# Optimization experiments

Measured on AMD Instinct MI355X. Metric: run time of the kernel, lower is better.

## Reference

```python
import jax, jax.numpy as jnp
import numpy as np

G = 2000      # number of genes
T = 64        # num_tf
NUM_GOS = 500
GO_DIM = 6
N_OUT = 7
B = 64        # batch (cells)


def _gene_layout():
    num_peaks = (np.arange(G) % 16) + 3          # ragged widths, total 21000
    gene_ids = np.repeat(np.arange(G), num_peaks).astype(np.int32)
    return num_peaks, gene_ids


def setup_inputs() -> dict:
    num_peaks, gene_ids = _gene_layout()
    P = int(num_peaks.sum())                     # 21000 total peaks
    key = jax.random.key(0)
    ks = jax.random.split(key, 7)
    x = jax.random.normal(ks[0], (B, T, P), dtype=jnp.float32)
    # per-peak-per-TF weights: concat of all subNet fc1 weights (each gene's
    # Linear(num_peak*num_tf, 1) is just a dot over its (tf, peak) block)
    W_peaks = jax.random.normal(ks[1], (P, T), dtype=jnp.float32) * 0.02
    b_genes = jax.random.normal(ks[2], (G,), dtype=jnp.float32) * 0.02
    W1 = jax.random.normal(ks[3], (G, NUM_GOS * GO_DIM), dtype=jnp.float32) * 0.02
    b1 = jax.random.normal(ks[4], (NUM_GOS * GO_DIM,), dtype=jnp.float32) * 0.02
    W2 = jax.random.normal(ks[5], (NUM_GOS * GO_DIM, N_OUT), dtype=jnp.float32) * 0.02
    b2 = jax.random.normal(ks[6], (N_OUT,), dtype=jnp.float32) * 0.02
    return {"x": x, "W_peaks": W_peaks, "b_genes": b_genes,
            "W1": W1, "b1": b1, "W2": W2, "b2": b2,
            "gene_ids": jnp.asarray(gene_ids)}


def reference(x, W_peaks, b_genes, W1, b1, W2, b2, gene_ids):
    # per-peak contribution: sum over TFs  -> [B, P]
    per_peak = jnp.einsum('btp,pt->bp', x, W_peaks)
    # ragged per-gene reduction (the subNet loop) -> [B, G]
    x_cat_pre = jax.ops.segment_sum(per_peak.T, gene_ids, num_segments=G).T + b_genes
    x_cat = jax.nn.relu(x_cat_pre)
    h = jax.nn.relu(x_cat @ W1 + b1)             # [B, num_gos*go_dim]
    out = h @ W2 + b2                            # [B, 7]
    return (x_cat, h, out)
```

## Files before the change

kernel.cpp:

```cpp
#include <hip/hip_runtime.h>

#define G_GENES 2000
#define T_TF    64
#define P_PEAKS 21000
#define B_BATCH 64
#define H_DIM   3000
#define N_OUT   7

#define WS_XCAT 0
#define WS_HACC 128000
#define WS_WT   320000


__global__ __launch_bounds__(256) void transpose_w(const float* __restrict__ W,
                                                   float* __restrict__ Wt) {
    __shared__ float tile[64][65];
    const int pBase = blockIdx.x * 64;
    const int tid = threadIdx.x;
    const int lane = tid & 63;
    const int grp  = tid >> 6;
#pragma unroll
    for (int i = 0; i < 16; ++i) {
        int pr = grp + i * 4;
        int p  = pBase + pr;
        if (p < P_PEAKS) tile[pr][lane] = W[(size_t)p * T_TF + lane];
    }
    __syncthreads();
#pragma unroll
    for (int i = 0; i < 16; ++i) {
        int tr = grp + i * 4;
        int p  = pBase + lane;
        if (p < P_PEAKS) Wt[(size_t)tr * P_PEAKS + p] = tile[lane][tr];
    }
}

__global__ __launch_bounds__(256) void peak_dot(const float* __restrict__ x,
                                                const float* __restrict__ Wt,
                                                const int*   __restrict__ gene_ids,
                                                float* __restrict__ xcat_acc) {
    const int p4 = blockIdx.x * 256 + threadIdx.x;
    if (p4 >= P_PEAKS / 4) return;
    const int b = blockIdx.y;
    const int p = p4 * 4;

    const float4* __restrict__ xp = (const float4*)(x + (size_t)b * T_TF * P_PEAKS + p);
    const float4* __restrict__ wp = (const float4*)(Wt + p);
    const int stride4 = P_PEAKS / 4;

    float4 acc = make_float4(0.f, 0.f, 0.f, 0.f);
#pragma unroll 8
    for (int t = 0; t < T_TF; ++t) {
        float4 xv = xp[(size_t)t * stride4];
        float4 wv = wp[(size_t)t * stride4];
        acc.x += xv.x * wv.x;
        acc.y += xv.y * wv.y;
        acc.z += xv.z * wv.z;
        acc.w += xv.w * wv.w;
    }

    const int4 g = *(const int4*)(gene_ids + p);
    float* dst = xcat_acc + (size_t)b * G_GENES;
    float s = acc.x; int cg = g.x;
    if (g.y == cg) s += acc.y; else { atomicAdd(dst + cg, s); cg = g.y; s = acc.y; }
    if (g.z == cg) s += acc.z; else { atomicAdd(dst + cg, s); cg = g.z; s = acc.z; }
    if (g.w == cg) s += acc.w; else { atomicAdd(dst + cg, s); cg = g.w; s = acc.w; }
    atomicAdd(dst + cg, s);
}

__global__ __launch_bounds__(256) void bias_relu_xcat(const float* __restrict__ acc,
                                                      const float* __restrict__ b_genes,
                                                      float* __restrict__ out) {
    int i = blockIdx.x * 256 + threadIdx.x;
    if (i >= B_BATCH * G_GENES) return;
    float v = acc[i] + b_genes[i % G_GENES];
    out[i] = v > 0.f ? v : 0.f;
}

#define KSPLIT 4
#define KCH    (2000 / KSPLIT)
#define KK_CH  20
__global__ __launch_bounds__(256) void gemm1(const float* __restrict__ A,
                                             const float* __restrict__ W1,
                                             float* __restrict__ h_acc) {
    __shared__ __align__(16) float As[KK_CH][64];
    const int tid = threadIdx.x;
    const int tx = tid & 15;
    const int ty = tid >> 4;
    const int colBase = blockIdx.x * 64;
    const int col0 = colBase + tx * 4;
    const int row0 = ty * 4;
    const int k0 = blockIdx.y * KCH;
    const bool colOK = (col0 < H_DIM);

    float4 acc4[4];
#pragma unroll
    for (int r = 0; r < 4; ++r) acc4[r] = make_float4(0.f, 0.f, 0.f, 0.f);

    for (int kc = 0; kc < KCH; kc += KK_CH) {
        __syncthreads();
#pragma unroll
        for (int i = 0; i < 5; ++i) {
            int idx = tid + i * 256;
            int kk = idx >> 6;
            int r  = idx & 63;
            As[kk][r] = A[(size_t)r * G_GENES + k0 + kc + kk];
        }
        __syncthreads();
        if (colOK) {
#pragma unroll
            for (int kk = 0; kk < KK_CH; ++kk) {
                float4 a4 = *(const float4*)&As[kk][row0];
                float4 w4 = *(const float4*)&W1[(size_t)(k0 + kc + kk) * H_DIM + col0];
                acc4[0].x += a4.x * w4.x; acc4[0].y += a4.x * w4.y;
                acc4[0].z += a4.x * w4.z; acc4[0].w += a4.x * w4.w;
                acc4[1].x += a4.y * w4.x; acc4[1].y += a4.y * w4.y;
                acc4[1].z += a4.y * w4.z; acc4[1].w += a4.y * w4.w;
                acc4[2].x += a4.z * w4.x; acc4[2].y += a4.z * w4.y;
                acc4[2].z += a4.z * w4.z; acc4[2].w += a4.z * w4.w;
                acc4[3].x += a4.w * w4.x; acc4[3].y += a4.w * w4.y;
                acc4[3].z += a4.w * w4.z; acc4[3].w += a4.w * w4.w;
            }
        }
    }
    if (colOK) {
#pragma unroll
        for (int r = 0; r < 4; ++r) {
            float* dst = h_acc + (size_t)(row0 + r) * H_DIM + col0;
            atomicAdd(dst + 0, acc4[r].x);
            atomicAdd(dst + 1, acc4[r].y);
            atomicAdd(dst + 2, acc4[r].z);
            atomicAdd(dst + 3, acc4[r].w);
        }
    }
}

__global__ __launch_bounds__(256) void bias_relu_h(const float* __restrict__ acc,
                                                   const float* __restrict__ b1,
                                                   float* __restrict__ out) {
    int i = blockIdx.x * 256 + threadIdx.x;
    if (i >= B_BATCH * H_DIM) return;
    float v = acc[i] + b1[i % H_DIM];
    out[i] = v > 0.f ? v : 0.f;
}

__global__ __launch_bounds__(256) void gemm2(const float* __restrict__ h,
                                             const float* __restrict__ W2,
                                             const float* __restrict__ b2,
                                             float* __restrict__ out) {
    const int b = blockIdx.x;
    const int tid = threadIdx.x;
    float acc[N_OUT];
#pragma unroll
    for (int o = 0; o < N_OUT; ++o) acc[o] = 0.f;
    for (int k = tid; k < H_DIM; k += 256) {
        float hv = h[(size_t)b * H_DIM + k];
#pragma unroll
        for (int o = 0; o < N_OUT; ++o) acc[o] += hv * W2[k * N_OUT + o];
    }
    __shared__ float red[N_OUT][256];
#pragma unroll
    for (int o = 0; o < N_OUT; ++o) red[o][tid] = acc[o];
    __syncthreads();
    for (int s = 128; s > 0; s >>= 1) {
        if (tid < s) {
#pragma unroll
            for (int o = 0; o < N_OUT; ++o) red[o][tid] += red[o][tid + s];
        }
        __syncthreads();
    }
    if (tid < N_OUT) out[(size_t)b * N_OUT + tid] = red[tid][0] + b2[tid];
}

extern "C" void kernel_launch(void* const* d_in, const int* in_sizes, int n_in,
                              void* d_out, int out_size, void* d_ws, size_t ws_size,
                              hipStream_t stream) {
    const float* x       = (const float*)d_in[0];
    const float* W_peaks = (const float*)d_in[1];
    const float* b_genes = (const float*)d_in[2];
    const float* W1      = (const float*)d_in[3];
    const float* b1      = (const float*)d_in[4];
    const float* W2      = (const float*)d_in[5];
    const float* b2      = (const float*)d_in[6];
    const int*   gene_ids = (const int*)d_in[7];

    float* ws = (float*)d_ws;
    float* xcat_acc = ws + WS_XCAT;
    float* h_acc    = ws + WS_HACC;
    float* Wt       = ws + WS_WT;

    float* out_xcat = (float*)d_out;
    float* out_h    = (float*)d_out + 128000;
    float* out_fin  = (float*)d_out + 320000;

    hipMemsetAsync(ws, 0, (size_t)(128000 + 192000) * sizeof(float), stream);

    transpose_w<<<(P_PEAKS + 63) / 64, 256, 0, stream>>>(W_peaks, Wt);

    dim3 g1((P_PEAKS / 4 + 255) / 256, B_BATCH);
    peak_dot<<<g1, 256, 0, stream>>>(x, Wt, gene_ids, xcat_acc);

    bias_relu_xcat<<<(B_BATCH * G_GENES + 255) / 256, 256, 0, stream>>>(
        xcat_acc, b_genes, out_xcat);

    dim3 g2((H_DIM + 63) / 64, KSPLIT);
    gemm1<<<g2, 256, 0, stream>>>(out_xcat, W1, h_acc);

    bias_relu_h<<<(B_BATCH * H_DIM + 255) / 256, 256, 0, stream>>>(
        h_acc, b1, out_h);

    gemm2<<<B_BATCH, 256, 0, stream>>>(out_h, W2, b2, out_fin);
}
```

Measured before the change: 573.5 us.

## Reuse W across 4 batches in peak_dot, transpose xcat for gemm1, raise K-split

peak_dot now gives each thread 4 batch rows, so each Wt load is reused four times and fewer blocks are launched. bias_relu_xcat also writes a transposed [G,B] copy of x_cat, which gives gemm1 coalesced shared-memory tile loads instead of strided ones. gemm1's K split goes from 4 to 8 with a 25-deep chunk, adding parallelism at the cost of more atomics on h_acc. The dominant cost is streaming x (about 344MB), so the W reuse mainly saves L2 traffic.

```diff
diff --git a/kernel.cpp b/kernel.cpp
--- a/kernel.cpp
+++ b/kernel.cpp
@@ -10,6 +10,7 @@
 #define WS_XCAT 0
 #define WS_HACC 128000
 #define WS_WT   320000
+#define WS_AT   (320000 + 1344000)
 
 
 __global__ __launch_bounds__(256) void transpose_w(const float* __restrict__ W,
@@ -34,60 +35,73 @@
     }
 }
 
-__global__ __launch_bounds__(256) void peak_dot(const float* __restrict__ x,
+__global__ __launch_bounds__(128) void peak_dot(const float* __restrict__ x,
                                                 const float* __restrict__ Wt,
                                                 const int*   __restrict__ gene_ids,
                                                 float* __restrict__ xcat_acc) {
-    const int p4 = blockIdx.x * 256 + threadIdx.x;
+    const int p4 = blockIdx.x * 128 + threadIdx.x;
     if (p4 >= P_PEAKS / 4) return;
-    const int b = blockIdx.y;
+    const int b0 = blockIdx.y * 4;
     const int p = p4 * 4;
-
-    const float4* __restrict__ xp = (const float4*)(x + (size_t)b * T_TF * P_PEAKS + p);
+    const int s4 = P_PEAKS / 4;
+
     const float4* __restrict__ wp = (const float4*)(Wt + p);
-    const int stride4 = P_PEAKS / 4;
-
-    float4 acc = make_float4(0.f, 0.f, 0.f, 0.f);
-#pragma unroll 8
+    const float4* __restrict__ xp = (const float4*)(x + (size_t)b0 * T_TF * P_PEAKS + p);
+
+    float4 acc[4];
+#pragma unroll
+    for (int bb = 0; bb < 4; ++bb) acc[bb] = make_float4(0.f, 0.f, 0.f, 0.f);
+
+#pragma unroll 4
     for (int t = 0; t < T_TF; ++t) {
-        float4 xv = xp[(size_t)t * stride4];
-        float4 wv = wp[(size_t)t * stride4];
-        acc.x += xv.x * wv.x;
-        acc.y += xv.y * wv.y;
-        acc.z += xv.z * wv.z;
-        acc.w += xv.w * wv.w;
+        float4 wv = wp[t * s4];
+#pragma unroll
+        for (int bb = 0; bb < 4; ++bb) {
+            float4 xv = xp[(bb * T_TF + t) * s4];
+            acc[bb].x += xv.x * wv.x;
+            acc[bb].y += xv.y * wv.y;
+            acc[bb].z += xv.z * wv.z;
+            acc[bb].w += xv.w * wv.w;
+        }
     }
 
     const int4 g = *(const int4*)(gene_ids + p);
-    float* dst = xcat_acc + (size_t)b * G_GENES;
-    float s = acc.x; int cg = g.x;
-    if (g.y == cg) s += acc.y; else { atomicAdd(dst + cg, s); cg = g.y; s = acc.y; }
-    if (g.z == cg) s += acc.z; else { atomicAdd(dst + cg, s); cg = g.z; s = acc.z; }
-    if (g.w == cg) s += acc.w; else { atomicAdd(dst + cg, s); cg = g.w; s = acc.w; }
-    atomicAdd(dst + cg, s);
+#pragma unroll
+    for (int bb = 0; bb < 4; ++bb) {
+        float* dst = xcat_acc + (size_t)(b0 + bb) * G_GENES;
+        float s = acc[bb].x; int cg = g.x;
+        if (g.y == cg) s += acc[bb].y; else { atomicAdd(dst + cg, s); cg = g.y; s = acc[bb].y; }
+        if (g.z == cg) s += acc[bb].z; else { atomicAdd(dst + cg, s); cg = g.z; s = acc[bb].z; }
+        if (g.w == cg) s += acc[bb].w; else { atomicAdd(dst + cg, s); cg = g.w; s = acc[bb].w; }
+        atomicAdd(dst + cg, s);
+    }
 }
 
 __global__ __launch_bounds__(256) void bias_relu_xcat(const float* __restrict__ acc,
                                                       const float* __restrict__ b_genes,
-                                                      float* __restrict__ out) {
+                                                      float* __restrict__ out,
+                                                      float* __restrict__ At) {
     int i = blockIdx.x * 256 + threadIdx.x;
     if (i >= B_BATCH * G_GENES) return;
-    float v = acc[i] + b_genes[i % G_GENES];
-    out[i] = v > 0.f ? v : 0.f;
-}
-
-#define KSPLIT 4
-#define KCH    (2000 / KSPLIT)
-#define KK_CH  20
-__global__ __launch_bounds__(256) void gemm1(const float* __restrict__ A,
+    int b = i / G_GENES;
+    int g = i - b * G_GENES;
+    float v = acc[i] + b_genes[g];
+    v = v > 0.f ? v : 0.f;
+    out[i] = v;
+    At[(size_t)g * B_BATCH + b] = v;
+}
+
+#define KSPLIT 8
+#define KCH    (G_GENES / KSPLIT)
+#define KK_CH  25
+__global__ __launch_bounds__(256) void gemm1(const float* __restrict__ At,
                                              const float* __restrict__ W1,
                                              float* __restrict__ h_acc) {
     __shared__ __align__(16) float As[KK_CH][64];
     const int tid = threadIdx.x;
     const int tx = tid & 15;
     const int ty = tid >> 4;
-    const int colBase = blockIdx.x * 64;
-    const int col0 = colBase + tx * 4;
+    const int col0 = blockIdx.x * 64 + tx * 4;
     const int row0 = ty * 4;
     const int k0 = blockIdx.y * KCH;
     const bool colOK = (col0 < H_DIM);
@@ -98,12 +112,10 @@
 
     for (int kc = 0; kc < KCH; kc += KK_CH) {
         __syncthreads();
-#pragma unroll
-        for (int i = 0; i < 5; ++i) {
-            int idx = tid + i * 256;
+        for (int idx = tid; idx < KK_CH * 64; idx += 256) {
             int kk = idx >> 6;
             int r  = idx & 63;
-            As[kk][r] = A[(size_t)r * G_GENES + k0 + kc + kk];
+            As[kk][r] = At[(size_t)(k0 + kc + kk) * B_BATCH + r];
         }
         __syncthreads();
         if (colOK) {
@@ -187,6 +199,7 @@
     float* xcat_acc = ws + WS_XCAT;
     float* h_acc    = ws + WS_HACC;
     float* Wt       = ws + WS_WT;
+    float* At       = ws + WS_AT;
 
     float* out_xcat = (float*)d_out;
     float* out_h    = (float*)d_out + 128000;
@@ -196,14 +209,14 @@
 
     transpose_w<<<(P_PEAKS + 63) / 64, 256, 0, stream>>>(W_peaks, Wt);
 
-    dim3 g1((P_PEAKS / 4 + 255) / 256, B_BATCH);
-    peak_dot<<<g1, 256, 0, stream>>>(x, Wt, gene_ids, xcat_acc);
+    dim3 g1((P_PEAKS / 4 + 127) / 128, B_BATCH / 4);
+    peak_dot<<<g1, 128, 0, stream>>>(x, Wt, gene_ids, xcat_acc);
 
     bias_relu_xcat<<<(B_BATCH * G_GENES + 255) / 256, 256, 0, stream>>>(
-        xcat_acc, b_genes, out_xcat);
+        xcat_acc, b_genes, out_xcat, At);
 
     dim3 g2((H_DIM + 63) / 64, KSPLIT);
-    gemm1<<<g2, 256, 0, stream>>>(out_xcat, W1, h_acc);
+    gemm1<<<g2, 256, 0, stream>>>(At, W1, h_acc);
 
     bias_relu_h<<<(B_BATCH * H_DIM + 255) / 256, 256, 0, stream>>>(
         h_acc, b1, out_h);
```

Measured after the change: 565.8 us. Within noise of the previous version (-1.3%).
